# Optimization experiments

Hardware: AMD Instinct MI355X
Metric: run time of the kernel (lower is better)

The kernel has to match this reference:

```python
import jax, jax.numpy as jnp
import numpy as np

N_VERTEX = 16384
D_IN = 64
HIDDEN = 64
D_OUT = 8
N_REGIONS = 64


def setup_inputs() -> dict:
    key = jax.random.key(0)
    ks = jax.random.split(key, 16)
    h = jax.random.normal(ks[0], (N_VERTEX, D_IN), dtype=jnp.float32)
    norm_adj = jax.random.uniform(ks[1], (N_VERTEX, N_VERTEX), dtype=jnp.float32) / N_VERTEX
    region_index = jax.random.randint(ks[2], (N_VERTEX,), 0, N_REGIONS, dtype=jnp.int32)
    s = 1.0 / np.sqrt(D_IN)
    W1 = jax.random.normal(ks[3], (D_IN, HIDDEN), dtype=jnp.float32) * s
    L1 = jax.random.normal(ks[4], (D_IN, HIDDEN), dtype=jnp.float32) * s
    rw1 = jax.random.normal(ks[5], (N_REGIONS, HIDDEN), dtype=jnp.float32) * 0.1 + 1.0
    rb1 = jax.random.normal(ks[6], (N_REGIONS, HIDDEN), dtype=jnp.float32) * 0.1
    sh = 1.0 / np.sqrt(HIDDEN)
    W2 = jax.random.normal(ks[7], (HIDDEN, HIDDEN), dtype=jnp.float32) * sh
    L2 = jax.random.normal(ks[8], (HIDDEN, HIDDEN), dtype=jnp.float32) * sh
    rw2 = jax.random.normal(ks[9], (N_REGIONS, HIDDEN), dtype=jnp.float32) * 0.1 + 1.0
    rb2 = jax.random.normal(ks[10], (N_REGIONS, HIDDEN), dtype=jnp.float32) * 0.1
    Wout = jax.random.normal(ks[11], (D_OUT, HIDDEN), dtype=jnp.float32) * sh
    bout = jax.random.normal(ks[12], (D_OUT,), dtype=jnp.float32) * 0.1
    return dict(h=h, norm_adj=norm_adj, region_index=region_index,
                W1=W1, L1=L1, rw1=rw1, rb1=rb1,
                W2=W2, L2=L2, rw2=rw2, rb2=rb2,
                Wout=Wout, bout=bout)


def _reg_conv(h, norm_adj, region_index, W, L, reg_w, reg_b):
    # ra = h @ W ; rb = norm_adj @ (h @ L)   [N, d_out]
    z = h @ W + norm_adj @ (h @ L)
    # per-vertex region gather of affine params (the irregular-access hot path)
    return z * reg_w[region_index] + reg_b[region_index]


def reference(h, norm_adj, region_index, W1, L1, rw1, rb1, W2, L2, rw2, rb2, Wout, bout):
    x = jax.nn.relu(_reg_conv(h, norm_adj, region_index, W1, L1, rw1, rb1))
    x = jax.nn.relu(_reg_conv(x, norm_adj, region_index, W2, L2, rw2, rb2))
    return x @ Wout.T + bout  # [N, d_out]
```

## Files before the change

kernel.cpp:

```cpp
#include <hip/hip_runtime.h>
#include <stdint.h>

#define NV 16384
#define BTQS (NV + 64)
#define BK 256
#define LDST8 272
#define NCH 16
#define SCUP 16384.0f
#define SCDN 6.103515625e-05f

typedef __attribute__((ext_vector_type(4))) float f32x4;

__global__ __launch_bounds__(256) void k_prep(
    const float* __restrict__ h, const float* __restrict__ W1,
    const float* __restrict__ L1, float* __restrict__ Z,
    unsigned char* __restrict__ Btq1) {
  __shared__ float Ws[4096], Ls[4096], hs[16 * 64];
  int tid = threadIdx.x;
  for (int i = tid; i < 4096; i += 256) { Ws[i] = W1[i]; Ls[i] = L1[i]; }
  int r = tid >> 6, c = tid & 63;
  int i0 = blockIdx.x << 4;
  #pragma unroll
  for (int m = 0; m < 4; ++m)
    hs[(r + 4 * m) * 64 + c] = h[(size_t)(i0 + r + 4 * m) * 64 + c];
  __syncthreads();
  float a1[4] = {0.f, 0.f, 0.f, 0.f};
  float a2[4] = {0.f, 0.f, 0.f, 0.f};
  #pragma unroll 8
  for (int k = 0; k < 64; ++k) {
    float wv = Ws[k * 64 + c];
    float lv = Ls[k * 64 + c];
    #pragma unroll
    for (int m = 0; m < 4; ++m) {
      float hv = hs[(r + 4 * m) * 64 + k];
      a1[m] += hv * wv;
      a2[m] += hv * lv;
    }
  }
  #pragma unroll
  for (int m = 0; m < 4; ++m) {
    int i = i0 + r + 4 * m;
    Z[(size_t)i * 64 + c] = a1[m];
    unsigned q = __builtin_amdgcn_cvt_pk_fp8_f32(a2[m], 0.0f, 0, false);
    Btq1[(size_t)c * BTQS + i] = (unsigned char)(q & 0xff);
  }
}

__global__ __launch_bounds__(256, 4) void k_adj1(
    const float* __restrict__ adj, const unsigned char* __restrict__ Btq,
    float* __restrict__ P, unsigned char* __restrict__ adj8) {
  __shared__ __align__(16) unsigned char Blds[2 * 64 * LDST8];
  const int tid = threadIdx.x;
  const int lane = tid & 63;
  const int w = tid >> 6;
  const int l15 = lane & 15;
  const int kgrp = lane >> 4;
  const int xb = blockIdx.x;
  const int yb = blockIdx.y;
  const int row = (xb << 6) + (w << 4) + l15;
  const int kbase = yb << 12;

  const int srow = tid >> 4;
  const int sc16 = tid & 15;
  const unsigned char* sbase = Btq + (size_t)srow * BTQS + kbase + sc16 * 16;
  unsigned char* lbase = Blds + srow * LDST8 + sc16 * 16;

  const float* ap = adj + (size_t)row * NV + kbase + kgrp * 8;
  unsigned char* a8w = adj8 +
      ((((size_t)xb * 4 + yb) * 4 + w) * 128) * 512 + (size_t)lane * 8;
  const int bofs0 = (l15 +  0) * LDST8 + kgrp * 8;
  const int bofs1 = (l15 + 16) * LDST8 + kgrp * 8;
  const int bofs2 = (l15 + 32) * LDST8 + kgrp * 8;
  const int bofs3 = (l15 + 48) * LDST8 + kgrp * 8;

  f32x4 sr0, sr1, sr2, sr3;
#define STAGE_LOAD8(KC)                                                  \
  { const unsigned char* s_ = sbase + (KC);                              \
    sr0 = *(const f32x4*)(s_);                                           \
    sr1 = *(const f32x4*)(s_ + (size_t)16 * BTQS);                       \
    sr2 = *(const f32x4*)(s_ + (size_t)32 * BTQS);                       \
    sr3 = *(const f32x4*)(s_ + (size_t)48 * BTQS); }
#define STAGE_WRITE8(BUF)                                                \
  { unsigned char* d_ = lbase + (BUF) * (64 * LDST8);                    \
    *(f32x4*)(d_) = sr0;                                                 \
    *(f32x4*)(d_ + 16 * LDST8) = sr1;                                    \
    *(f32x4*)(d_ + 32 * LDST8) = sr2;                                    \
    *(f32x4*)(d_ + 48 * LDST8) = sr3; }

  f32x4 aj0a, aj0b, aj1a, aj1b, aj2a, aj2b, aj3a, aj3b;

  STAGE_LOAD8(0);
  aj0a = *(const f32x4*)(ap +   0); aj0b = *(const f32x4*)(ap +   4);
  aj1a = *(const f32x4*)(ap +  32); aj1b = *(const f32x4*)(ap +  36);
  aj2a = *(const f32x4*)(ap +  64); aj2b = *(const f32x4*)(ap +  68);
  aj3a = *(const f32x4*)(ap +  96); aj3b = *(const f32x4*)(ap + 100);
  STAGE_WRITE8(0);
  __syncthreads();

  f32x4 acc0 = {0.f, 0.f, 0.f, 0.f};
  f32x4 acc1 = {0.f, 0.f, 0.f, 0.f};
  f32x4 acc2 = {0.f, 0.f, 0.f, 0.f};
  f32x4 acc3 = {0.f, 0.f, 0.f, 0.f};

#define ITER1(II, AJA, AJB)                                              \
  {                                                                      \
    unsigned pk0 = __builtin_amdgcn_cvt_pk_fp8_f32(AJA[0] * SCUP, AJA[1] * SCUP, 0, false); \
    pk0 = __builtin_amdgcn_cvt_pk_fp8_f32(AJA[2] * SCUP, AJA[3] * SCUP, pk0, true);         \
    unsigned pk1 = __builtin_amdgcn_cvt_pk_fp8_f32(AJB[0] * SCUP, AJB[1] * SCUP, 0, false); \
    pk1 = __builtin_amdgcn_cvt_pk_fp8_f32(AJB[2] * SCUP, AJB[3] * SCUP, pk1, true);         \
    unsigned long long av = (unsigned long long)pk0 | ((unsigned long long)pk1 << 32); \
    *(unsigned long long*)(a8w + (size_t)((t << 3) + (II)) * 512) = av;  \
    long long a_ = (long long)av;                                        \
    int ci = ((t << 3) + (II) + 4) & 127;                                \
    AJA = *(const f32x4*)(ap + (size_t)ci * 32);                         \
    AJB = *(const f32x4*)(ap + (size_t)ci * 32 + 4);                     \
    long long b0 = *(const long long*)(bb + bofs0 + (II) * 32);          \
    long long b1 = *(const long long*)(bb + bofs1 + (II) * 32);          \
    long long b2 = *(const long long*)(bb + bofs2 + (II) * 32);          \
    long long b3 = *(const long long*)(bb + bofs3 + (II) * 32);          \
    acc0 = __builtin_amdgcn_mfma_f32_16x16x32_fp8_fp8(a_, b0, acc0, 0, 0, 0); \
    acc1 = __builtin_amdgcn_mfma_f32_16x16x32_fp8_fp8(a_, b1, acc1, 0, 0, 0); \
    acc2 = __builtin_amdgcn_mfma_f32_16x16x32_fp8_fp8(a_, b2, acc2, 0, 0, 0); \
    acc3 = __builtin_amdgcn_mfma_f32_16x16x32_fp8_fp8(a_, b3, acc3, 0, 0, 0); \
  }

  for (int t = 0; t < NCH; ++t) {
    const unsigned char* bb = Blds + (t & 1) * (64 * LDST8);
    if (t + 1 < NCH) STAGE_LOAD8((t + 1) * BK);
    ITER1(0, aj0a, aj0b)
    ITER1(1, aj1a, aj1b)
    ITER1(2, aj2a, aj2b)
    ITER1(3, aj3a, aj3b)
    ITER1(4, aj0a, aj0b)
    ITER1(5, aj1a, aj1b)
    ITER1(6, aj2a, aj2b)
    ITER1(7, aj3a, aj3b)
    if (t + 1 < NCH) STAGE_WRITE8((t + 1) & 1);
    __syncthreads();
  }

  int zr = (xb << 6) + (w << 4) + (kgrp << 2);
  float* pp = P + (size_t)yb * NV * 64 + (size_t)zr * 64 + l15;
  #pragma unroll
  for (int r = 0; r < 4; ++r) {
    pp[(size_t)r * 64 +  0] = acc0[r] * SCDN;
    pp[(size_t)r * 64 + 16] = acc1[r] * SCDN;
    pp[(size_t)r * 64 + 32] = acc2[r] * SCDN;
    pp[(size_t)r * 64 + 48] = acc3[r] * SCDN;
  }
#undef ITER1
}

__global__ __launch_bounds__(256, 4) void k_adj8(
    const unsigned char* __restrict__ adj8, const unsigned char* __restrict__ Btq,
    float* __restrict__ P) {
  __shared__ __align__(16) unsigned char Blds[2 * 64 * LDST8];
  const int tid = threadIdx.x;
  const int lane = tid & 63;
  const int w = tid >> 6;
  const int l15 = lane & 15;
  const int kgrp = lane >> 4;
  const int xb = blockIdx.x;
  const int yb = blockIdx.y;
  const int kbase = yb << 12;

  const int srow = tid >> 4;
  const int sc16 = tid & 15;
  const unsigned char* sbase = Btq + (size_t)srow * BTQS + kbase + sc16 * 16;
  unsigned char* lbase = Blds + srow * LDST8 + sc16 * 16;

  const unsigned char* ap8 = adj8 +
      ((((size_t)xb * 4 + yb) * 4 + w) * 128) * 512 + (size_t)lane * 8;
  const int bofs0 = (l15 +  0) * LDST8 + kgrp * 8;
  const int bofs1 = (l15 + 16) * LDST8 + kgrp * 8;
  const int bofs2 = (l15 + 32) * LDST8 + kgrp * 8;
  const int bofs3 = (l15 + 48) * LDST8 + kgrp * 8;

  f32x4 sr0, sr1, sr2, sr3;

  unsigned long long aj0, aj1, aj2, aj3;

  STAGE_LOAD8(0);
  aj0 = *(const unsigned long long*)(ap8 +    0);
  aj1 = *(const unsigned long long*)(ap8 +  512);
  aj2 = *(const unsigned long long*)(ap8 + 1024);
  aj3 = *(const unsigned long long*)(ap8 + 1536);
  STAGE_WRITE8(0);
  __syncthreads();

  f32x4 acc0 = {0.f, 0.f, 0.f, 0.f};
  f32x4 acc1 = {0.f, 0.f, 0.f, 0.f};
  f32x4 acc2 = {0.f, 0.f, 0.f, 0.f};
  f32x4 acc3 = {0.f, 0.f, 0.f, 0.f};

#define ITER8(II, AJ)                                                    \
  {                                                                      \
    long long a_ = (long long)AJ;                                        \
    int ci = ((t << 3) + (II) + 4) & 127;                                \
    AJ = *(const unsigned long long*)(ap8 + (size_t)ci * 512);           \
    long long b0 = *(const long long*)(bb + bofs0 + (II) * 32);          \
    long long b1 = *(const long long*)(bb + bofs1 + (II) * 32);          \
    long long b2 = *(const long long*)(bb + bofs2 + (II) * 32);          \
    long long b3 = *(const long long*)(bb + bofs3 + (II) * 32);          \
    acc0 = __builtin_amdgcn_mfma_f32_16x16x32_fp8_fp8(a_, b0, acc0, 0, 0, 0); \
    acc1 = __builtin_amdgcn_mfma_f32_16x16x32_fp8_fp8(a_, b1, acc1, 0, 0, 0); \
    acc2 = __builtin_amdgcn_mfma_f32_16x16x32_fp8_fp8(a_, b2, acc2, 0, 0, 0); \
    acc3 = __builtin_amdgcn_mfma_f32_16x16x32_fp8_fp8(a_, b3, acc3, 0, 0, 0); \
  }

  for (int t = 0; t < NCH; ++t) {
    const unsigned char* bb = Blds + (t & 1) * (64 * LDST8);
    if (t + 1 < NCH) STAGE_LOAD8((t + 1) * BK);
    ITER8(0, aj0)
    ITER8(1, aj1)
    ITER8(2, aj2)
    ITER8(3, aj3)
    ITER8(4, aj0)
    ITER8(5, aj1)
    ITER8(6, aj2)
    ITER8(7, aj3)
    if (t + 1 < NCH) STAGE_WRITE8((t + 1) & 1);
    __syncthreads();
  }

  int zr = (xb << 6) + (w << 4) + (kgrp << 2);
  float* pp = P + (size_t)yb * NV * 64 + (size_t)zr * 64 + l15;
  #pragma unroll
  for (int r = 0; r < 4; ++r) {
    pp[(size_t)r * 64 +  0] = acc0[r] * SCDN;
    pp[(size_t)r * 64 + 16] = acc1[r] * SCDN;
    pp[(size_t)r * 64 + 32] = acc2[r] * SCDN;
    pp[(size_t)r * 64 + 48] = acc3[r] * SCDN;
  }
#undef ITER8
#undef STAGE_LOAD8
#undef STAGE_WRITE8
}

__global__ __launch_bounds__(256) void k_mid(
    float* __restrict__ Z, const float* __restrict__ P,
    const int* __restrict__ reg,
    const float* __restrict__ rw1, const float* __restrict__ rb1,
    const float* __restrict__ W2, const float* __restrict__ L2,
    unsigned char* __restrict__ Btq2) {
  __shared__ float Ws[4096], Ls[4096], xs[16 * 64];
  int tid = threadIdx.x;
  for (int i = tid; i < 4096; i += 256) { Ws[i] = W2[i]; Ls[i] = L2[i]; }
  int r = tid >> 6, c = tid & 63;
  int i0 = blockIdx.x << 4;
  #pragma unroll
  for (int m = 0; m < 4; ++m) {
    int i = i0 + r + 4 * m;
    int ri = reg[i];
    size_t o = (size_t)i * 64 + c;
    float z = Z[o] + P[o] + P[(size_t)NV * 64 + o] +
              P[(size_t)2 * NV * 64 + o] + P[(size_t)3 * NV * 64 + o];
    float x = z * rw1[ri * 64 + c] + rb1[ri * 64 + c];
    xs[(r + 4 * m) * 64 + c] = fmaxf(x, 0.f);
  }
  __syncthreads();
  float a1[4] = {0.f, 0.f, 0.f, 0.f};
  float a2[4] = {0.f, 0.f, 0.f, 0.f};
  #pragma unroll 8
  for (int k = 0; k < 64; ++k) {
    float wv = Ws[k * 64 + c];
    float lv = Ls[k * 64 + c];
    #pragma unroll
    for (int m = 0; m < 4; ++m) {
      float xv = xs[(r + 4 * m) * 64 + k];
      a1[m] += xv * wv;
      a2[m] += xv * lv;
    }
  }
  #pragma unroll
  for (int m = 0; m < 4; ++m) {
    int i = i0 + r + 4 * m;
    Z[(size_t)i * 64 + c] = a1[m];
    unsigned q = __builtin_amdgcn_cvt_pk_fp8_f32(a2[m], 0.0f, 0, false);
    Btq2[(size_t)c * BTQS + i] = (unsigned char)(q & 0xff);
  }
}

__global__ __launch_bounds__(256) void k_out(
    const float* __restrict__ Z, const float* __restrict__ P,
    const int* __restrict__ reg,
    const float* __restrict__ rw2, const float* __restrict__ rb2,
    const float* __restrict__ Wout, const float* __restrict__ bout,
    float* __restrict__ out) {
  __shared__ float xs[16 * 64];
  int tid = threadIdx.x;
  int r = tid >> 6, c = tid & 63;
  int i0 = blockIdx.x << 4;
  #pragma unroll
  for (int m = 0; m < 4; ++m) {
    int i = i0 + r + 4 * m;
    int ri = reg[i];
    size_t o = (size_t)i * 64 + c;
    float z = Z[o] + P[o] + P[(size_t)NV * 64 + o] +
              P[(size_t)2 * NV * 64 + o] + P[(size_t)3 * NV * 64 + o];
    float x = z * rw2[ri * 64 + c] + rb2[ri * 64 + c];
    xs[(r + 4 * m) * 64 + c] = fmaxf(x, 0.f);
  }
  __syncthreads();
  if (c < 8) {
    #pragma unroll
    for (int m = 0; m < 4; ++m) {
      int i = i0 + r + 4 * m;
      float a = bout[c];
      #pragma unroll 8
      for (int k = 0; k < 64; ++k) a += xs[(r + 4 * m) * 64 + k] * Wout[c * 64 + k];
      out[(size_t)i * 8 + c] = a;
    }
  }
}

extern "C" void kernel_launch(void* const* d_in, const int* in_sizes, int n_in,
                              void* d_out, int out_size, void* d_ws, size_t ws_size,
                              hipStream_t stream) {
  const float* h    = (const float*)d_in[0];
  const float* adj  = (const float*)d_in[1];
  const int*   reg  = (const int*)d_in[2];
  const float* W1   = (const float*)d_in[3];
  const float* L1   = (const float*)d_in[4];
  const float* rw1  = (const float*)d_in[5];
  const float* rb1  = (const float*)d_in[6];
  const float* W2   = (const float*)d_in[7];
  const float* L2   = (const float*)d_in[8];
  const float* rw2  = (const float*)d_in[9];
  const float* rb2  = (const float*)d_in[10];
  const float* Wout = (const float*)d_in[11];
  const float* bout = (const float*)d_in[12];
  float* out = (float*)d_out;

  char* ws = (char*)d_ws;
  float* Z            = (float*)(ws);
  unsigned char* Btq1 = (unsigned char*)(ws + ((size_t)4  << 20));
  float* P            = (float*)(ws + ((size_t)8  << 20));
  unsigned char* Btq2 = (unsigned char*)(ws + ((size_t)24 << 20));
  unsigned char* adj8 = (unsigned char*)(ws + ((size_t)28 << 20));

  k_prep<<<NV / 16, 256, 0, stream>>>(h, W1, L1, Z, Btq1);
  k_adj1<<<dim3(NV / 64, 4), 256, 0, stream>>>(adj, Btq1, P, adj8);
  k_mid<<<NV / 16, 256, 0, stream>>>(Z, P, reg, rw1, rb1, W2, L2, Btq2);
  k_adj8<<<dim3(NV / 64, 4), 256, 0, stream>>>(adj8, Btq2, P);
  k_out<<<NV / 16, 256, 0, stream>>>(Z, P, reg, rw2, rb2, Wout, bout, out);
}
```

Baseline: 395.5 us.

## Split K into 16 slices and stage whole B slice in LDS once

Raises the split-K factor of both adjacency GEMMs from 4 to 16, so each block handles a 1024-wide K slice and the grid grows from 1024 to 4096 blocks. Each block now copies its whole fp8 B slice into LDS up front, which removes the per-chunk double buffering and the syncthreads inside the loop. It also keeps 8 A loads in flight instead of 4. In exchange, the LDS footprint grows (occupancy hint lowered to 2), and 16 partial-sum planes must be written and then re-read in k_mid and k_out, raising their memory traffic.

```diff
diff --git a/kernel.cpp b/kernel.cpp
--- a/kernel.cpp
+++ b/kernel.cpp
@@ -3,9 +3,10 @@
 
 #define NV 16384
 #define BTQS (NV + 64)
-#define BK 256
-#define LDST8 272
-#define NCH 16
+#define NSP 16
+#define KSL 1024
+#define NIT 32
+#define LDSTR 1040
 #define SCUP 16384.0f
 #define SCDN 6.103515625e-05f
 
@@ -46,10 +47,21 @@
   }
 }
 
-__global__ __launch_bounds__(256, 4) void k_adj1(
+#define STAGE_SLICE(BLDS, BTQ, KB)                                       \
+  {                                                                      \
+    _Pragma("unroll")                                                    \
+    for (int j = 0; j < 16; ++j) {                                       \
+      int u = tid + j * 256;                                             \
+      int r_ = u >> 6, c16 = u & 63;                                     \
+      *(f32x4*)(BLDS + r_ * LDSTR + c16 * 16) =                          \
+          *(const f32x4*)(BTQ + (size_t)r_ * BTQS + (KB) + c16 * 16);    \
+    }                                                                    \
+  }
+
+__global__ __launch_bounds__(256, 2) void k_adj1(
     const float* __restrict__ adj, const unsigned char* __restrict__ Btq,
     float* __restrict__ P, unsigned char* __restrict__ adj8) {
-  __shared__ __align__(16) unsigned char Blds[2 * 64 * LDST8];
+  __shared__ __align__(16) unsigned char Blds[64 * LDSTR];
   const int tid = threadIdx.x;
   const int lane = tid & 63;
   const int w = tid >> 6;
@@ -58,44 +70,30 @@
   const int xb = blockIdx.x;
   const int yb = blockIdx.y;
   const int row = (xb << 6) + (w << 4) + l15;
-  const int kbase = yb << 12;
-
-  const int srow = tid >> 4;
-  const int sc16 = tid & 15;
-  const unsigned char* sbase = Btq + (size_t)srow * BTQS + kbase + sc16 * 16;
-  unsigned char* lbase = Blds + srow * LDST8 + sc16 * 16;
+  const int kbase = yb << 10;
+
+  STAGE_SLICE(Blds, Btq, kbase)
 
   const float* ap = adj + (size_t)row * NV + kbase + kgrp * 8;
   unsigned char* a8w = adj8 +
-      ((((size_t)xb * 4 + yb) * 4 + w) * 128) * 512 + (size_t)lane * 8;
-  const int bofs0 = (l15 +  0) * LDST8 + kgrp * 8;
-  const int bofs1 = (l15 + 16) * LDST8 + kgrp * 8;
-  const int bofs2 = (l15 + 32) * LDST8 + kgrp * 8;
-  const int bofs3 = (l15 + 48) * LDST8 + kgrp * 8;
-
-  f32x4 sr0, sr1, sr2, sr3;
-#define STAGE_LOAD8(KC)                                                  \
-  { const unsigned char* s_ = sbase + (KC);                              \
-    sr0 = *(const f32x4*)(s_);                                           \
-    sr1 = *(const f32x4*)(s_ + (size_t)16 * BTQS);                       \
-    sr2 = *(const f32x4*)(s_ + (size_t)32 * BTQS);                       \
-    sr3 = *(const f32x4*)(s_ + (size_t)48 * BTQS); }
-#define STAGE_WRITE8(BUF)                                                \
-  { unsigned char* d_ = lbase + (BUF) * (64 * LDST8);                    \
-    *(f32x4*)(d_) = sr0;                                                 \
-    *(f32x4*)(d_ + 16 * LDST8) = sr1;                                    \
-    *(f32x4*)(d_ + 32 * LDST8) = sr2;                                    \
-    *(f32x4*)(d_ + 48 * LDST8) = sr3; }
+      ((((size_t)xb * NSP + yb) * 4 + w) * NIT) * 512 + (size_t)lane * 8;
+  const int bofs0 = (l15 +  0) * LDSTR + kgrp * 8;
+  const int bofs1 = (l15 + 16) * LDSTR + kgrp * 8;
+  const int bofs2 = (l15 + 32) * LDSTR + kgrp * 8;
+  const int bofs3 = (l15 + 48) * LDSTR + kgrp * 8;
+
+  __syncthreads();
 
   f32x4 aj0a, aj0b, aj1a, aj1b, aj2a, aj2b, aj3a, aj3b;
-
-  STAGE_LOAD8(0);
+  f32x4 aj4a, aj4b, aj5a, aj5b, aj6a, aj6b, aj7a, aj7b;
   aj0a = *(const f32x4*)(ap +   0); aj0b = *(const f32x4*)(ap +   4);
   aj1a = *(const f32x4*)(ap +  32); aj1b = *(const f32x4*)(ap +  36);
   aj2a = *(const f32x4*)(ap +  64); aj2b = *(const f32x4*)(ap +  68);
   aj3a = *(const f32x4*)(ap +  96); aj3b = *(const f32x4*)(ap + 100);
-  STAGE_WRITE8(0);
-  __syncthreads();
+  aj4a = *(const f32x4*)(ap + 128); aj4b = *(const f32x4*)(ap + 132);
+  aj5a = *(const f32x4*)(ap + 160); aj5b = *(const f32x4*)(ap + 164);
+  aj6a = *(const f32x4*)(ap + 192); aj6b = *(const f32x4*)(ap + 196);
+  aj7a = *(const f32x4*)(ap + 224); aj7b = *(const f32x4*)(ap + 228);
 
   f32x4 acc0 = {0.f, 0.f, 0.f, 0.f};
   f32x4 acc1 = {0.f, 0.f, 0.f, 0.f};
@@ -111,7 +109,7 @@
     unsigned long long av = (unsigned long long)pk0 | ((unsigned long long)pk1 << 32); \
     *(unsigned long long*)(a8w + (size_t)((t << 3) + (II)) * 512) = av;  \
     long long a_ = (long long)av;                                        \
-    int ci = ((t << 3) + (II) + 4) & 127;                                \
+    int ci = ((t << 3) + (II) + 8) & (NIT - 1);                          \
     AJA = *(const f32x4*)(ap + (size_t)ci * 32);                         \
     AJB = *(const f32x4*)(ap + (size_t)ci * 32 + 4);                     \
     long long b0 = *(const long long*)(bb + bofs0 + (II) * 32);          \
@@ -124,19 +122,16 @@
     acc3 = __builtin_amdgcn_mfma_f32_16x16x32_fp8_fp8(a_, b3, acc3, 0, 0, 0); \
   }
 
-  for (int t = 0; t < NCH; ++t) {
-    const unsigned char* bb = Blds + (t & 1) * (64 * LDST8);
-    if (t + 1 < NCH) STAGE_LOAD8((t + 1) * BK);
+  for (int t = 0; t < NIT / 8; ++t) {
+    const unsigned char* bb = Blds + t * 256;
     ITER1(0, aj0a, aj0b)
     ITER1(1, aj1a, aj1b)
     ITER1(2, aj2a, aj2b)
     ITER1(3, aj3a, aj3b)
-    ITER1(4, aj0a, aj0b)
-    ITER1(5, aj1a, aj1b)
-    ITER1(6, aj2a, aj2b)
-    ITER1(7, aj3a, aj3b)
-    if (t + 1 < NCH) STAGE_WRITE8((t + 1) & 1);
-    __syncthreads();
+    ITER1(4, aj4a, aj4b)
+    ITER1(5, aj5a, aj5b)
+    ITER1(6, aj6a, aj6b)
+    ITER1(7, aj7a, aj7b)
   }
 
   int zr = (xb << 6) + (w << 4) + (kgrp << 2);
@@ -151,10 +146,10 @@
 #undef ITER1
 }
 
-__global__ __launch_bounds__(256, 4) void k_adj8(
+__global__ __launch_bounds__(256, 2) void k_adj8(
     const unsigned char* __restrict__ adj8, const unsigned char* __restrict__ Btq,
     float* __restrict__ P) {
-  __shared__ __align__(16) unsigned char Blds[2 * 64 * LDST8];
+  __shared__ __align__(16) unsigned char Blds[64 * LDSTR];
   const int tid = threadIdx.x;
   const int lane = tid & 63;
   const int w = tid >> 6;
@@ -162,31 +157,28 @@
   const int kgrp = lane >> 4;
   const int xb = blockIdx.x;
   const int yb = blockIdx.y;
-  const int kbase = yb << 12;
-
-  const int srow = tid >> 4;
-  const int sc16 = tid & 15;
-  const unsigned char* sbase = Btq + (size_t)srow * BTQS + kbase + sc16 * 16;
-  unsigned char* lbase = Blds + srow * LDST8 + sc16 * 16;
+  const int kbase = yb << 10;
+
+  STAGE_SLICE(Blds, Btq, kbase)
 
   const unsigned char* ap8 = adj8 +
-      ((((size_t)xb * 4 + yb) * 4 + w) * 128) * 512 + (size_t)lane * 8;
-  const int bofs0 = (l15 +  0) * LDST8 + kgrp * 8;
-  const int bofs1 = (l15 + 16) * LDST8 + kgrp * 8;
-  const int bofs2 = (l15 + 32) * LDST8 + kgrp * 8;
-  const int bofs3 = (l15 + 48) * LDST8 + kgrp * 8;
-
-  f32x4 sr0, sr1, sr2, sr3;
-
-  unsigned long long aj0, aj1, aj2, aj3;
-
-  STAGE_LOAD8(0);
+      ((((size_t)xb * NSP + yb) * 4 + w) * NIT) * 512 + (size_t)lane * 8;
+  const int bofs0 = (l15 +  0) * LDSTR + kgrp * 8;
+  const int bofs1 = (l15 + 16) * LDSTR + kgrp * 8;
+  const int bofs2 = (l15 + 32) * LDSTR + kgrp * 8;
+  const int bofs3 = (l15 + 48) * LDSTR + kgrp * 8;
+
+  __syncthreads();
+
+  unsigned long long aj0, aj1, aj2, aj3, aj4, aj5, aj6, aj7;
   aj0 = *(const unsigned long long*)(ap8 +    0);
   aj1 = *(const unsigned long long*)(ap8 +  512);
   aj2 = *(const unsigned long long*)(ap8 + 1024);
   aj3 = *(const unsigned long long*)(ap8 + 1536);
-  STAGE_WRITE8(0);
-  __syncthreads();
+  aj4 = *(const unsigned long long*)(ap8 + 2048);
+  aj5 = *(const unsigned long long*)(ap8 + 2560);
+  aj6 = *(const unsigned long long*)(ap8 + 3072);
+  aj7 = *(const unsigned long long*)(ap8 + 3584);
 
   f32x4 acc0 = {0.f, 0.f, 0.f, 0.f};
   f32x4 acc1 = {0.f, 0.f, 0.f, 0.f};
@@ -196,7 +188,7 @@
 #define ITER8(II, AJ)                                                    \
   {                                                                      \
     long long a_ = (long long)AJ;                                        \
-    int ci = ((t << 3) + (II) + 4) & 127;                                \
+    int ci = ((t << 3) + (II) + 8) & (NIT - 1);                          \
     AJ = *(const unsigned long long*)(ap8 + (size_t)ci * 512);           \
     long long b0 = *(const long long*)(bb + bofs0 + (II) * 32);          \
     long long b1 = *(const long long*)(bb + bofs1 + (II) * 32);          \
@@ -208,19 +200,16 @@
     acc3 = __builtin_amdgcn_mfma_f32_16x16x32_fp8_fp8(a_, b3, acc3, 0, 0, 0); \
   }
 
-  for (int t = 0; t < NCH; ++t) {
-    const unsigned char* bb = Blds + (t & 1) * (64 * LDST8);
-    if (t + 1 < NCH) STAGE_LOAD8((t + 1) * BK);
+  for (int t = 0; t < NIT / 8; ++t) {
+    const unsigned char* bb = Blds + t * 256;
     ITER8(0, aj0)
     ITER8(1, aj1)
     ITER8(2, aj2)
     ITER8(3, aj3)
-    ITER8(4, aj0)
-    ITER8(5, aj1)
-    ITER8(6, aj2)
-    ITER8(7, aj3)
-    if (t + 1 < NCH) STAGE_WRITE8((t + 1) & 1);
-    __syncthreads();
+    ITER8(4, aj4)
+    ITER8(5, aj5)
+    ITER8(6, aj6)
+    ITER8(7, aj7)
   }
 
   int zr = (xb << 6) + (w << 4) + (kgrp << 2);
@@ -233,8 +222,6 @@
     pp[(size_t)r * 64 + 48] = acc3[r] * SCDN;
   }
 #undef ITER8
-#undef STAGE_LOAD8
-#undef STAGE_WRITE8
 }
 
 __global__ __launch_bounds__(256) void k_mid(
@@ -253,8 +240,9 @@
     int i = i0 + r + 4 * m;
     int ri = reg[i];
     size_t o = (size_t)i * 64 + c;
-    float z = Z[o] + P[o] + P[(size_t)NV * 64 + o] +
-              P[(size_t)2 * NV * 64 + o] + P[(size_t)3 * NV * 64 + o];
+    float z = Z[o];
+    #pragma unroll
+    for (int j = 0; j < NSP; ++j) z += P[(size_t)j * NV * 64 + o];
     float x = z * rw1[ri * 64 + c] + rb1[ri * 64 + c];
     xs[(r + 4 * m) * 64 + c] = fmaxf(x, 0.f);
   }
@@ -296,8 +284,9 @@
     int i = i0 + r + 4 * m;
     int ri = reg[i];
     size_t o = (size_t)i * 64 + c;
-    float z = Z[o] + P[o] + P[(size_t)NV * 64 + o] +
-              P[(size_t)2 * NV * 64 + o] + P[(size_t)3 * NV * 64 + o];
+    float z = Z[o];
+    #pragma unroll
+    for (int j = 0; j < NSP; ++j) z += P[(size_t)j * NV * 64 + o];
     float x = z * rw2[ri * 64 + c] + rb2[ri * 64 + c];
     xs[(r + 4 * m) * 64 + c] = fmaxf(x, 0.f);
   }
@@ -336,12 +325,12 @@
   float* Z            = (float*)(ws);
   unsigned char* Btq1 = (unsigned char*)(ws + ((size_t)4  << 20));
   float* P            = (float*)(ws + ((size_t)8  << 20));
-  unsigned char* Btq2 = (unsigned char*)(ws + ((size_t)24 << 20));
-  unsigned char* adj8 = (unsigned char*)(ws + ((size_t)28 << 20));
+  unsigned char* Btq2 = (unsigned char*)(ws + ((size_t)76 << 20));
+  unsigned char* adj8 = (unsigned char*)(ws + ((size_t)80 << 20));
 
   k_prep<<<NV / 16, 256, 0, stream>>>(h, W1, L1, Z, Btq1);
-  k_adj1<<<dim3(NV / 64, 4), 256, 0, stream>>>(adj, Btq1, P, adj8);
+  k_adj1<<<dim3(NV / 64, NSP), 256, 0, stream>>>(adj, Btq1, P, adj8);
   k_mid<<<NV / 16, 256, 0, stream>>>(Z, P, reg, rw1, rb1, W2, L2, Btq2);
-  k_adj8<<<dim3(NV / 64, 4), 256, 0, stream>>>(adj8, Btq2, P);
+  k_adj8<<<dim3(NV / 64, NSP), 256, 0, stream>>>(adj8, Btq2, P);
   k_out<<<NV / 16, 256, 0, stream>>>(Z, P, reg, rw2, rb2, Wout, bout, out);
 }
```

Result: slower. 429.1 us (+8.5%).
